# Kernel optimization log

Hardware: AMD Instinct MI355X
Metric: run time of the kernel (lower is better)

The kernel has to match this reference:

```python
import jax, jax.numpy as jnp
import numpy as np

TEMPERATURE = 0.5
EPS = 1e-08
N, D = 8192, 128

def setup_inputs() -> dict:
    key = jax.random.key(0)
    k1, k2 = jax.random.split(key)
    labels = jax.random.randint(k1, (N,), 0, 3, dtype=jnp.int64 if jax.config.jax_enable_x64 else jnp.int32) - 1  # values in {-1,0,1}
    embeddings = jax.random.normal(k2, (N, D), dtype=jnp.float32)
    return {"labels": labels, "embeddings": embeddings}

def reference(labels, embeddings):
    n = embeddings.shape[0]
    lz = labels == 0                              # [N] nodes with label 0
    same = labels[:, None] == labels[None, :]     # [N,N]
    # nonzero-label anchors: positives are same label or label==0 targets;
    # zero-label anchors: positives are all nodes with label in {-1,0,1} (i.e. all)
    pos = jnp.where(lz[:, None], True, same | lz[None, :])
    diag = jnp.eye(n, dtype=bool)
    pos = pos & ~diag
    neg = (~pos) & ~diag
    pos_f = pos.astype(embeddings.dtype)
    neg_f = neg.astype(embeddings.dtype)

    sim = (embeddings @ embeddings.T) / TEMPERATURE            # [N,N]
    sim = sim - jax.lax.stop_gradient(jnp.max(sim, axis=1, keepdims=True))
    exp_sim = jnp.exp(sim)
    pos_sim = jnp.sum(pos_f * exp_sim, axis=1)
    neg_sim = jnp.sum(neg_f * exp_sim, axis=1)

    valid = jnp.sum(pos_f, axis=1) > 0
    loss = -jnp.log((pos_sim + EPS) / (pos_sim + neg_sim + EPS))
    count = jnp.sum(valid)
    mean_loss = jnp.sum(jnp.where(valid, loss, 0.0)) / jnp.maximum(count, 1)
    return jnp.where(count > 0, mean_loss, 0.0)
```

## Files before the change

### kernel.cpp

```cpp
#include <hip/hip_runtime.h>


#define NROWS 8192
#define DDIM  128
#define EPSV  1e-8f
#define SCALE 1.69864368f

#define BN     32
#define ROWB   64
#define CSPLIT 16
#define CPB    (NROWS / CSPLIT)
#define NT     (CPB / BN)

typedef short bf16x8 __attribute__((ext_vector_type(8)));
typedef float f32x4  __attribute__((ext_vector_type(4)));
typedef int   i32x4  __attribute__((ext_vector_type(4)));
typedef unsigned short u16;
typedef unsigned int   u32;
typedef unsigned long long u64;

__device__ __forceinline__ u16 f2bf(float f) {
  u32 u = __float_as_uint(f);
  u32 r = u + 0x7fffu + ((u >> 16) & 1u);
  return (u16)(r >> 16);
}
__device__ __forceinline__ float bf2f(u16 h) {
  return __uint_as_float(((u32)h) << 16);
}
__device__ __forceinline__ float exp2x(float x) {
#if __has_builtin(__builtin_amdgcn_exp2f)
  return __builtin_amdgcn_exp2f(x);
#else
  return exp2f(x);
#endif
}

__global__ __launch_bounds__(256) void prep_kernel(
    const float* __restrict__ emb, const int* __restrict__ labels,
    u16* __restrict__ ehi, float* __restrict__ mrow, u32* __restrict__ maxn,
    int* __restrict__ cnt) {
  __shared__ float wmax[4];
  const int tid = blockIdx.x * 256 + threadIdx.x;
  const float4* src = ((const float4*)emb) + (size_t)tid * 2;
  float4 a = src[0], b = src[1];
  float v[8] = {a.x, a.y, a.z, a.w, b.x, b.y, b.z, b.w};
  union { u16 us[8]; bf16x8 v8; } hv;
  float s2 = 0.f;
#pragma unroll
  for (int i = 0; i < 8; ++i) {
    float f  = v[i] * SCALE;
    u16 hb   = f2bf(f);
    hv.us[i] = hb;
    const float hr = bf2f(hb);
    s2 = fmaf(hr, hr, s2);
  }
  *(bf16x8*)(ehi + (size_t)tid * 8) = hv.v8;
  s2 += __shfl_xor(s2, 1);
  s2 += __shfl_xor(s2, 2);
  s2 += __shfl_xor(s2, 4);
  s2 += __shfl_xor(s2, 8);
  if ((tid & 15) == 0) mrow[tid >> 4] = sqrtf(s2);

  float ms2 = s2;
  ms2 = fmaxf(ms2, __shfl_xor(ms2, 16));
  ms2 = fmaxf(ms2, __shfl_xor(ms2, 32));
  if ((threadIdx.x & 63) == 0) wmax[threadIdx.x >> 6] = ms2;
  __syncthreads();
  if (threadIdx.x == 0) {
    const float m = fmaxf(fmaxf(wmax[0], wmax[1]), fmaxf(wmax[2], wmax[3]));
    atomicMax(maxn, __float_as_uint(sqrtf(m)));
  }

  if (tid < NROWS) {
    const int li = labels[tid];
    const u64 b_m1 = __ballot(li == -1);
    const u64 b_z  = __ballot(li == 0);
    if ((threadIdx.x & 63) == 0) {
      const int n_m1 = __popcll(b_m1);
      const int n_z  = __popcll(b_z);
      atomicAdd(&cnt[0], n_m1);
      atomicAdd(&cnt[1], n_z);
      atomicAdd(&cnt[2], 64 - n_m1 - n_z);
    }
  }
}

__global__ __launch_bounds__(256) void sim_kernel(
    const u16* __restrict__ ehi, const int* __restrict__ labels,
    const float* __restrict__ mrow, const u32* __restrict__ maxn,
    float* __restrict__ ps, float* __restrict__ pp) {

  __shared__ __align__(16) u16 lhi[2][BN * DDIM];
  __shared__ __align__(16) int llab[2][BN];

  const int tid  = threadIdx.x;
  const int lane = tid & 63;
  const int l15  = lane & 15;
  const int lq   = lane >> 4;
  const int wave = tid >> 6;

  const int wrow0 = blockIdx.x * ROWB + wave * 16;
  const int col0  = blockIdx.y * CPB;

  bf16x8 rh[4];
  {
    const u16* bh = ehi + (size_t)(wrow0 + l15) * DDIM + lq * 8;
#pragma unroll
    for (int kc = 0; kc < 4; ++kc) rh[kc] = *(const bf16x8*)(bh + kc * 32);
  }

  const int li0  = labels[wrow0 + l15];
  const int nli0 = -li0;
  const float m0 = mrow[wrow0 + l15] * __uint_as_float(*maxn);

  const int c0    = tid >> 4;
  const int slot  = tid & 15;
  const u32 d0    = ((u32)(tid * 16)) ^ ((u32)((c0 & 15) << 4));
  const int goff0 = c0 * DDIM + slot * 8;
  const int goff1 = goff0 + 16 * DDIM;

  const u32 swzb  = (u32)(l15 << 4);
  const u32 rbase = (u32)(l15 * 256 + lq * 16);

  float S0 = 0.f, P0 = 0.f;

  bf16x8 gh0, gh1;
  int glab = 0;

  {
    gh0 = *(const bf16x8*)(ehi + (size_t)col0 * DDIM + goff0);
    gh1 = *(const bf16x8*)(ehi + (size_t)col0 * DDIM + goff1);
    if (tid < BN) glab = labels[col0 + tid];
    *(bf16x8*)((char*)(&lhi[0][0]) + d0)         = gh0;
    *(bf16x8*)((char*)(&lhi[0][0]) + d0 + 4096u) = gh1;
    if (tid < BN) llab[0][tid] = glab;
  }
  __syncthreads();

  int bufi = 0;
#pragma unroll 1
  for (int t = 0; t < NT; ++t) {
    const int cb = col0 + t * BN;
    const bool hasnext = (t + 1 < NT);
    if (hasnext) {
      const int cbn = cb + BN;
      gh0 = *(const bf16x8*)(ehi + (size_t)cbn * DDIM + goff0);
      gh1 = *(const bf16x8*)(ehi + (size_t)cbn * DDIM + goff1);
      if (tid < BN) glab = labels[cbn + tid];
    }

    const char* ph = (const char*)(&lhi[bufi][0]);
    const i32x4 labq0 = *(const i32x4*)(&llab[bufi][lq * 4]);
    const i32x4 labq1 = *(const i32x4*)(&llab[bufi][16 + lq * 4]);

    f32x4 acc0 = {-m0, -m0, -m0, -m0};
    f32x4 acc1 = {-m0, -m0, -m0, -m0};

    __builtin_amdgcn_s_setprio(1);
#pragma unroll
    for (int kc = 0; kc < 4; ++kc) {
      const u32 o0 = (rbase + (u32)(kc * 64)) ^ swzb;
      const bf16x8 ah0 = *(const bf16x8*)(ph + o0);
      const bf16x8 ah1 = *(const bf16x8*)(ph + o0 + 4096u);
      acc0 = __builtin_amdgcn_mfma_f32_16x16x32_bf16(ah0, rh[kc], acc0, 0, 0, 0);
      acc1 = __builtin_amdgcn_mfma_f32_16x16x32_bf16(ah1, rh[kc], acc1, 0, 0, 0);
    }
    __builtin_amdgcn_s_setprio(0);

    const bool dt0 = (cb == wrow0);
    const bool dt1 = (cb + 16 == wrow0);
    if (!dt0 && !dt1) {
#pragma unroll
      for (int q = 0; q < 4; ++q) {
        const float e0 = exp2x(acc0[q]);
        const float e1 = exp2x(acc1[q]);
        S0 += e0 + e1;
        P0 += (labq0[q] != nli0 ? e0 : 0.f) + (labq1[q] != nli0 ? e1 : 0.f);
      }
    } else if (dt0) {
#pragma unroll
      for (int q = 0; q < 4; ++q) {
        const bool dd = (lq * 4 + q == l15);
        const float e0 = dd ? 0.f : exp2x(acc0[q]);
        const float e1 = exp2x(acc1[q]);
        S0 += e0 + e1;
        P0 += (labq0[q] != nli0 ? e0 : 0.f) + (labq1[q] != nli0 ? e1 : 0.f);
      }
    } else {
#pragma unroll
      for (int q = 0; q < 4; ++q) {
        const float e0 = exp2x(acc0[q]);
        const bool dd = (lq * 4 + q == l15);
        const float e1 = dd ? 0.f : exp2x(acc1[q]);
        S0 += e0 + e1;
        P0 += (labq0[q] != nli0 ? e0 : 0.f) + (labq1[q] != nli0 ? e1 : 0.f);
      }
    }

    if (hasnext) {
      char* wh = (char*)(&lhi[bufi ^ 1][0]);
      *(bf16x8*)(wh + d0)         = gh0;
      *(bf16x8*)(wh + d0 + 4096u) = gh1;
      if (tid < BN) llab[bufi ^ 1][tid] = glab;
    }
    __syncthreads();
    bufi ^= 1;
  }

  if (li0 == 0) P0 = S0;

  S0 += __shfl_xor(S0, 16); P0 += __shfl_xor(P0, 16);
  S0 += __shfl_xor(S0, 32); P0 += __shfl_xor(P0, 32);

  if (lane < 16) {
    const int base = (int)blockIdx.y * NROWS + wrow0 + l15;
    ps[base] = S0; pp[base] = P0;
  }
}

__global__ __launch_bounds__(256) void merge_kernel(
    const float* __restrict__ ps, const float* __restrict__ pp,
    const int* __restrict__ labels, const int* __restrict__ cnt,
    float* __restrict__ acc) {
  const int i = blockIdx.x * 256 + threadIdx.x;
  float S = 0.f, P = 0.f;
#pragma unroll
  for (int c = 0; c < CSPLIT; ++c) {
    S += ps[c * NROWS + i];
    P += pp[c * NROWS + i];
  }
  const int li = labels[i];
  const int pcnt = (li == 0) ? (NROWS - 1) : (cnt[li + 1] - 1 + cnt[1]);
  const bool valid = pcnt > 0;
  float loss = valid ? (-__logf((P + EPSV) / (S + EPSV))) : 0.f;
  float vc   = valid ? 1.f : 0.f;
#pragma unroll
  for (int off = 32; off > 0; off >>= 1) {
    loss += __shfl_down(loss, off);
    vc   += __shfl_down(vc, off);
  }
  if ((threadIdx.x & 63) == 0) {
    atomicAdd(&acc[0], loss);
    atomicAdd(&acc[1], vc);
  }
}

__global__ void final_kernel(const float* __restrict__ acc, float* __restrict__ out) {
  if (threadIdx.x == 0 && blockIdx.x == 0) {
    const float c = acc[1];
    out[0] = (c > 0.f) ? (acc[0] / c) : 0.f;
  }
}

extern "C" void kernel_launch(void* const* d_in, const int* in_sizes, int n_in,
                              void* d_out, int out_size, void* d_ws, size_t ws_size,
                              hipStream_t stream) {
  (void)in_sizes; (void)n_in; (void)out_size; (void)ws_size;
  const int*   labels = (const int*)d_in[0];
  const float* emb    = (const float*)d_in[1];

  char* ws = (char*)d_ws;
  u16*   ehi  = (u16*)(ws);
  float* mrow = (float*)(ws + (size_t)NROWS * DDIM * 2);
  float* ps   = mrow + NROWS;
  float* pp   = ps + CSPLIT * NROWS;
  int*   cnt  = (int*)(pp + CSPLIT * NROWS);
  float* acc  = (float*)(cnt + 4);
  u32*   maxn = (u32*)(acc + 2);

  hipMemsetAsync(cnt, 0, 28, stream);
  prep_kernel<<<NROWS * DDIM / 8 / 256, 256, 0, stream>>>(emb, labels, ehi, mrow, maxn, cnt);
  sim_kernel<<<dim3(NROWS / ROWB, CSPLIT), 256, 0, stream>>>(ehi, labels, mrow, maxn, ps, pp);
  merge_kernel<<<NROWS / 256, 256, 0, stream>>>(ps, pp, labels, cnt, acc);
  final_kernel<<<1, 64, 0, stream>>>(acc, (float*)d_out);
}
```

Measured before the change: 109.2 us.

## Drop LDS staging of column tiles and compute two row tiles per wave

```diff
diff --git a/kernel.cpp b/kernel.cpp
--- a/kernel.cpp
+++ b/kernel.cpp
@@ -7,7 +7,7 @@
 #define SCALE 1.69864368f
 
 #define BN     32
-#define ROWB   64
+#define ROWB   128
 #define CSPLIT 16
 #define CPB    (NROWS / CSPLIT)
 #define NT     (CPB / BN)
@@ -90,8 +90,7 @@
     const float* __restrict__ mrow, const u32* __restrict__ maxn,
     float* __restrict__ ps, float* __restrict__ pp) {
 
-  __shared__ __align__(16) u16 lhi[2][BN * DDIM];
-  __shared__ __align__(16) int llab[2][BN];
+  __shared__ __align__(16) int llab[CPB];
 
   const int tid  = threadIdx.x;
   const int lane = tid & 63;
@@ -99,122 +98,100 @@
   const int lq   = lane >> 4;
   const int wave = tid >> 6;
 
-  const int wrow0 = blockIdx.x * ROWB + wave * 16;
+  const int wrow0 = blockIdx.x * ROWB + wave * 32;
   const int col0  = blockIdx.y * CPB;
 
-  bf16x8 rh[4];
-  {
-    const u16* bh = ehi + (size_t)(wrow0 + l15) * DDIM + lq * 8;
-#pragma unroll
-    for (int kc = 0; kc < 4; ++kc) rh[kc] = *(const bf16x8*)(bh + kc * 32);
+  llab[tid]       = labels[col0 + tid];
+  llab[tid + 256] = labels[col0 + tid + 256];
+
+  bf16x8 rh[2][4];
+#pragma unroll
+  for (int rt = 0; rt < 2; ++rt) {
+    const u16* bh = ehi + (size_t)(wrow0 + rt * 16 + l15) * DDIM + lq * 8;
+#pragma unroll
+    for (int kc = 0; kc < 4; ++kc) rh[rt][kc] = *(const bf16x8*)(bh + kc * 32);
   }
 
   const int li0  = labels[wrow0 + l15];
-  const int nli0 = -li0;
-  const float m0 = mrow[wrow0 + l15] * __uint_as_float(*maxn);
-
-  const int c0    = tid >> 4;
-  const int slot  = tid & 15;
-  const u32 d0    = ((u32)(tid * 16)) ^ ((u32)((c0 & 15) << 4));
-  const int goff0 = c0 * DDIM + slot * 8;
-  const int goff1 = goff0 + 16 * DDIM;
-
-  const u32 swzb  = (u32)(l15 << 4);
-  const u32 rbase = (u32)(l15 * 256 + lq * 16);
-
-  float S0 = 0.f, P0 = 0.f;
-
-  bf16x8 gh0, gh1;
-  int glab = 0;
-
-  {
-    gh0 = *(const bf16x8*)(ehi + (size_t)col0 * DDIM + goff0);
-    gh1 = *(const bf16x8*)(ehi + (size_t)col0 * DDIM + goff1);
-    if (tid < BN) glab = labels[col0 + tid];
-    *(bf16x8*)((char*)(&lhi[0][0]) + d0)         = gh0;
-    *(bf16x8*)((char*)(&lhi[0][0]) + d0 + 4096u) = gh1;
-    if (tid < BN) llab[0][tid] = glab;
-  }
+  const int li1  = labels[wrow0 + 16 + l15];
+  const int nli0 = -li0, nli1 = -li1;
+  const float mxn = __uint_as_float(*maxn);
+  const float m0 = mrow[wrow0 + l15] * mxn;
+  const float m1 = mrow[wrow0 + 16 + l15] * mxn;
+
   __syncthreads();
 
-  int bufi = 0;
+  float S0 = 0.f, P0 = 0.f, S1 = 0.f, P1 = 0.f;
+
 #pragma unroll 1
   for (int t = 0; t < NT; ++t) {
     const int cb = col0 + t * BN;
-    const bool hasnext = (t + 1 < NT);
-    if (hasnext) {
-      const int cbn = cb + BN;
-      gh0 = *(const bf16x8*)(ehi + (size_t)cbn * DDIM + goff0);
-      gh1 = *(const bf16x8*)(ehi + (size_t)cbn * DDIM + goff1);
-      if (tid < BN) glab = labels[cbn + tid];
-    }
-
-    const char* ph = (const char*)(&lhi[bufi][0]);
-    const i32x4 labq0 = *(const i32x4*)(&llab[bufi][lq * 4]);
-    const i32x4 labq1 = *(const i32x4*)(&llab[bufi][16 + lq * 4]);
-
-    f32x4 acc0 = {-m0, -m0, -m0, -m0};
-    f32x4 acc1 = {-m0, -m0, -m0, -m0};
+
+    const u16* ac = ehi + (size_t)(cb + l15) * DDIM + lq * 8;
+    bf16x8 ah0[4], ah1[4];
+#pragma unroll
+    for (int kc = 0; kc < 4; ++kc) {
+      ah0[kc] = *(const bf16x8*)(ac + kc * 32);
+      ah1[kc] = *(const bf16x8*)(ac + 16 * DDIM + kc * 32);
+    }
+    const i32x4 labq0 = *(const i32x4*)(&llab[t * BN + lq * 4]);
+    const i32x4 labq1 = *(const i32x4*)(&llab[t * BN + 16 + lq * 4]);
+
+    f32x4 accA0 = {-m0, -m0, -m0, -m0};
+    f32x4 accA1 = {-m1, -m1, -m1, -m1};
+    f32x4 accB0 = {-m0, -m0, -m0, -m0};
+    f32x4 accB1 = {-m1, -m1, -m1, -m1};
 
     __builtin_amdgcn_s_setprio(1);
 #pragma unroll
     for (int kc = 0; kc < 4; ++kc) {
-      const u32 o0 = (rbase + (u32)(kc * 64)) ^ swzb;
-      const bf16x8 ah0 = *(const bf16x8*)(ph + o0);
-      const bf16x8 ah1 = *(const bf16x8*)(ph + o0 + 4096u);
-      acc0 = __builtin_amdgcn_mfma_f32_16x16x32_bf16(ah0, rh[kc], acc0, 0, 0, 0);
-      acc1 = __builtin_amdgcn_mfma_f32_16x16x32_bf16(ah1, rh[kc], acc1, 0, 0, 0);
+      accA0 = __builtin_amdgcn_mfma_f32_16x16x32_bf16(ah0[kc], rh[0][kc], accA0, 0, 0, 0);
+      accA1 = __builtin_amdgcn_mfma_f32_16x16x32_bf16(ah0[kc], rh[1][kc], accA1, 0, 0, 0);
+      accB0 = __builtin_amdgcn_mfma_f32_16x16x32_bf16(ah1[kc], rh[0][kc], accB0, 0, 0, 0);
+      accB1 = __builtin_amdgcn_mfma_f32_16x16x32_bf16(ah1[kc], rh[1][kc], accB1, 0, 0, 0);
     }
     __builtin_amdgcn_s_setprio(0);
 
-    const bool dt0 = (cb == wrow0);
-    const bool dt1 = (cb + 16 == wrow0);
-    if (!dt0 && !dt1) {
+    if (cb != wrow0) {
 #pragma unroll
       for (int q = 0; q < 4; ++q) {
-        const float e0 = exp2x(acc0[q]);
-        const float e1 = exp2x(acc1[q]);
-        S0 += e0 + e1;
-        P0 += (labq0[q] != nli0 ? e0 : 0.f) + (labq1[q] != nli0 ? e1 : 0.f);
+        const float eA0 = exp2x(accA0[q]);
+        const float eB0 = exp2x(accB0[q]);
+        S0 += eA0 + eB0;
+        P0 += (labq0[q] != nli0 ? eA0 : 0.f) + (labq1[q] != nli0 ? eB0 : 0.f);
+        const float eA1 = exp2x(accA1[q]);
+        const float eB1 = exp2x(accB1[q]);
+        S1 += eA1 + eB1;
+        P1 += (labq0[q] != nli1 ? eA1 : 0.f) + (labq1[q] != nli1 ? eB1 : 0.f);
       }
-    } else if (dt0) {
+    } else {
 #pragma unroll
       for (int q = 0; q < 4; ++q) {
         const bool dd = (lq * 4 + q == l15);
-        const float e0 = dd ? 0.f : exp2x(acc0[q]);
-        const float e1 = exp2x(acc1[q]);
-        S0 += e0 + e1;
-        P0 += (labq0[q] != nli0 ? e0 : 0.f) + (labq1[q] != nli0 ? e1 : 0.f);
+        const float eA0 = dd ? 0.f : exp2x(accA0[q]);
+        const float eB0 = exp2x(accB0[q]);
+        S0 += eA0 + eB0;
+        P0 += (labq0[q] != nli0 ? eA0 : 0.f) + (labq1[q] != nli0 ? eB0 : 0.f);
+        const float eA1 = exp2x(accA1[q]);
+        const float eB1 = dd ? 0.f : exp2x(accB1[q]);
+        S1 += eA1 + eB1;
+        P1 += (labq0[q] != nli1 ? eA1 : 0.f) + (labq1[q] != nli1 ? eB1 : 0.f);
       }
-    } else {
-#pragma unroll
-      for (int q = 0; q < 4; ++q) {
-        const float e0 = exp2x(acc0[q]);
-        const bool dd = (lq * 4 + q == l15);
-        const float e1 = dd ? 0.f : exp2x(acc1[q]);
-        S0 += e0 + e1;
-        P0 += (labq0[q] != nli0 ? e0 : 0.f) + (labq1[q] != nli0 ? e1 : 0.f);
-      }
-    }
-
-    if (hasnext) {
-      char* wh = (char*)(&lhi[bufi ^ 1][0]);
-      *(bf16x8*)(wh + d0)         = gh0;
-      *(bf16x8*)(wh + d0 + 4096u) = gh1;
-      if (tid < BN) llab[bufi ^ 1][tid] = glab;
-    }
-    __syncthreads();
-    bufi ^= 1;
+    }
   }
 
   if (li0 == 0) P0 = S0;
+  if (li1 == 0) P1 = S1;
 
   S0 += __shfl_xor(S0, 16); P0 += __shfl_xor(P0, 16);
   S0 += __shfl_xor(S0, 32); P0 += __shfl_xor(P0, 32);
+  S1 += __shfl_xor(S1, 16); P1 += __shfl_xor(P1, 16);
+  S1 += __shfl_xor(S1, 32); P1 += __shfl_xor(P1, 32);
 
   if (lane < 16) {
     const int base = (int)blockIdx.y * NROWS + wrow0 + l15;
-    ps[base] = S0; pp[base] = P0;
+    ps[base] = S0;      pp[base] = P0;
+    ps[base + 16] = S1; pp[base + 16] = P1;
   }
 }
 
```

Result: slower. 141.6 us (+29.7%).
